# Kernel tuning notes

Measured on AMD Instinct MI355X. Metric: run time of the kernel, lower is better.

## Reference

```python
import jax, jax.numpy as jnp
import numpy as np

V = 500_000
NF = 1_000_000
K_DEG = 7


def _build_mesh_ops(rng):
    faces = rng.integers(0, V, size=(NF, 3), dtype=np.int64)
    f0, f1, f2 = faces[:, 0], faces[:, 1], faces[:, 2]
    rows = np.concatenate([f0, f1, f1, f2, f2, f0])
    cols = np.concatenate([f1, f0, f2, f1, f0, f2])
    keep = rows != cols
    rows, cols = rows[keep], cols[keep]
    code = np.unique(rows * V + cols)  # dedupe symmetric edge list
    rows_u = (code // V).astype(np.int32)
    cols_u = (code % V).astype(np.int32)
    deg = np.bincount(rows_u, minlength=V).astype(np.float32)
    deg = np.maximum(deg, 1.0)
    off_vals = (1.0 / deg[rows_u]).astype(np.float32)
    diag = np.arange(V, dtype=np.int32)
    lap_rows = np.concatenate([rows_u, diag])
    lap_cols = np.concatenate([cols_u, diag])
    lap_vals = np.concatenate([off_vals, -np.ones(V, dtype=np.float32)])
    # sparse hexagon operator K: ~7 nnz per row
    k_rows = np.repeat(np.arange(V, dtype=np.int32), K_DEG)
    k_cols = rng.integers(0, V, size=V * K_DEG).astype(np.int32)
    k_vals = (rng.standard_normal(V * K_DEG) * 0.1).astype(np.float32)
    return faces.astype(np.int32), lap_rows, lap_cols, lap_vals, k_rows, k_cols, k_vals


def setup_inputs() -> dict:
    key = jax.random.key(0)
    rng = np.random.default_rng(0)
    faces, lap_rows, lap_cols, lap_vals, k_rows, k_cols, k_vals = _build_mesh_ops(rng)
    vertices = jax.random.normal(key, (V, 3), dtype=jnp.float32)
    return {
        "vertices": vertices,
        "center": jnp.zeros((1, 3), dtype=jnp.float32),
        "lap_rows": jnp.asarray(lap_rows),
        "lap_cols": jnp.asarray(lap_cols),
        "lap_vals": jnp.asarray(lap_vals),
        "k_rows": jnp.asarray(k_rows),
        "k_cols": jnp.asarray(k_cols),
        "k_vals": jnp.asarray(k_vals),
        "faces": jnp.asarray(faces),
        "total_num": 4,
    }


def _spmv3(rows, cols, vals, verts, n):
    # sparse [n,n] COO matmul with [n,3] verts
    gathered = vals[:, None] * verts[cols]  # [nnz,3]
    return jax.ops.segment_sum(gathered, rows, num_segments=n)


def reference(vertices, center, lap_rows, lap_cols, lap_vals,
              k_rows, k_cols, k_vals, faces, total_num):
    n = vertices.shape[0]
    verts = vertices + center  # [V,3], broadcast of [1,3] center
    # uniform laplacian smoothing loss: mean_i ||(L v)_i||_2
    lap_out = _spmv3(lap_rows, lap_cols, lap_vals, verts, n)
    laplacian_loss = jnp.mean(jnp.linalg.norm(lap_out, axis=1))
    # hexagon regularity loss: mean_i ||(K v)_i||^2
    k_out = _spmv3(k_rows, k_cols, k_vals, verts, n)
    hexagon_loss = jnp.mean(jnp.sum(k_out * k_out, axis=1))
    vertices_rep = jnp.tile(verts[None], (total_num, 1, 1))
    faces_rep = jnp.tile(faces[None], (total_num, 1, 1))
    zero = jnp.zeros((), dtype=verts.dtype)
    return (vertices_rep, faces_rep, laplacian_loss, hexagon_loss, zero, zero)
```

## Files before the change

kernel.cpp:

```cpp
#include <hip/hip_runtime.h>
#include <hip/hip_fp16.h>
#include <math.h>

#define BLK  256
#define KDEG 7
#define CH   8

typedef float fvec4 __attribute__((ext_vector_type(4)));
typedef int   ivec4 __attribute__((ext_vector_type(4)));

__global__ void vrep_kernel(const fvec4* __restrict__ vin,
                            const float* __restrict__ center,
                            fvec4* __restrict__ out,
                            int n4, int T) {
    int i = blockIdx.x * blockDim.x + threadIdx.x;
    if (i >= n4) return;
    float c0 = center[0], c1 = center[1], c2 = center[2];
    fvec4 f = vin[i];
    int m = i % 3;
    float a0 = (m == 0) ? c0 : (m == 1) ? c1 : c2;
    float a1 = (m == 0) ? c1 : (m == 1) ? c2 : c0;
    float a2 = (m == 0) ? c2 : (m == 1) ? c0 : c1;
    f.x += a0; f.y += a1; f.z += a2; f.w += a0;
    for (int t = 0; t < T; ++t)
        __builtin_nontemporal_store(f, &out[(long)t * n4 + i]);
}

__global__ void pack_kernel(const float* __restrict__ vertices,
                            const float* __restrict__ center,
                            ushort4* __restrict__ v16,
                            int* __restrict__ row_start,
                            float* __restrict__ out, long scalar_base, int V) {
    int r = blockIdx.x * blockDim.x + threadIdx.x;
    if (r == 0) {
        out[scalar_base + 0] = 0.f;
        out[scalar_base + 1] = 0.f;
        out[scalar_base + 2] = 0.f;
        out[scalar_base + 3] = 0.f;
    }
    if (r >= V) return;
    long b = (long)r * 3;
    float x = vertices[b]     + center[0];
    float y = vertices[b + 1] + center[1];
    float z = vertices[b + 2] + center[2];
    ushort4 u;
    u.x = __half_as_ushort(__float2half(x));
    u.y = __half_as_ushort(__float2half(y));
    u.z = __half_as_ushort(__float2half(z));
    u.w = 0;
    v16[r] = u;
    row_start[r] = -1;
}

__global__ void frep_kernel(const ivec4* __restrict__ faces,
                            fvec4* __restrict__ out,
                            int n4, int T) {
    int i = blockIdx.x * blockDim.x + threadIdx.x;
    if (i >= n4) return;
    ivec4 f = faces[i];
    fvec4 g;
    g.x = (float)f.x; g.y = (float)f.y; g.z = (float)f.z; g.w = (float)f.w;
    for (int t = 0; t < T; ++t)
        __builtin_nontemporal_store(g, &out[(long)t * n4 + i]);
}

__global__ void row_bounds_kernel(const int* __restrict__ rows,
                                  int* __restrict__ row_start,
                                  int* __restrict__ row_end,
                                  int nnz_off) {
    int j = blockIdx.x * blockDim.x + threadIdx.x;
    if (j >= nnz_off) return;
    int r = rows[j];
    if (j == 0) {
        row_start[r] = 0;
    } else {
        int rp = rows[j - 1];
        if (rp != r) {
            row_start[r] = j;
            row_end[rp] = j;
        }
    }
    if (j == nnz_off - 1) row_end[r] = nnz_off;
}

__device__ __forceinline__ float2 block_reduce_sum2(float2 v) {
    for (int o = 32; o > 0; o >>= 1) {
        v.x += __shfl_down(v.x, o, 64);
        v.y += __shfl_down(v.y, o, 64);
    }
    __shared__ float2 s[BLK / 64];
    int lane = threadIdx.x & 63;
    int wid  = threadIdx.x >> 6;
    if (lane == 0) s[wid] = v;
    __syncthreads();
    if (wid == 0) {
        v = (lane < BLK / 64) ? s[lane] : make_float2(0.f, 0.f);
        for (int o = (BLK / 64) / 2; o > 0; o >>= 1) {
            v.x += __shfl_down(v.x, o, 64);
            v.y += __shfl_down(v.y, o, 64);
        }
    }
    return v;
}

__launch_bounds__(BLK, 6)
__global__ void fused_loss_kernel(const int* __restrict__ row_start,
                                  const int* __restrict__ row_end,
                                  const int* __restrict__ cols,
                                  const int* __restrict__ kcols,
                                  const float* __restrict__ kvals,
                                  const ushort4* __restrict__ v16,
                                  int V, float invV,
                                  float* __restrict__ acc ) {
    const int r   = blockIdx.x * BLK + threadIdx.x;
    const bool act = (r < V);
    const int rr  = act ? r : 0;

    int lo = 0, hi = 0;
    if (act) {
        lo = row_start[r];
        hi = (lo >= 0) ? row_end[r] : 0;
        if (lo < 0) lo = 0;
    }
    const int cnt = hi - lo;

    float qx = 0.f, qy = 0.f, qz = 0.f;
    {
        long kb = (long)rr * KDEG;
        int   kc[KDEG]; float kv[KDEG];
#pragma unroll
        for (int t = 0; t < KDEG; ++t) { kc[t] = kcols[kb + t]; kv[t] = kvals[kb + t]; }
        ushort4 ku[KDEG];
#pragma unroll
        for (int t = 0; t < KDEG; ++t) ku[t] = v16[kc[t]];
#pragma unroll
        for (int t = 0; t < KDEG; ++t) {
            qx += kv[t] * __half2float(__ushort_as_half(ku[t].x));
            qy += kv[t] * __half2float(__ushort_as_half(ku[t].y));
            qz += kv[t] * __half2float(__ushort_as_half(ku[t].z));
        }
    }

    float sx = 0.f, sy = 0.f, sz = 0.f;
    for (int j = lo; j < hi; j += CH) {
        int m = hi - j; if (m > CH) m = CH;
        int cc[CH];
#pragma unroll
        for (int t = 0; t < CH; ++t)
            if (t < m) cc[t] = cols[j + t];
        ushort4 cu[CH];
#pragma unroll
        for (int t = 0; t < CH; ++t)
            if (t < m) cu[t] = v16[cc[t]];
#pragma unroll
        for (int t = 0; t < CH; ++t)
            if (t < m) {
                sx += __half2float(__ushort_as_half(cu[t].x));
                sy += __half2float(__ushort_as_half(cu[t].y));
                sz += __half2float(__ushort_as_half(cu[t].z));
            }
    }

    float2 contrib = make_float2(0.f, 0.f);
    if (act) {
        ushort4 ur = v16[rr];
        float vx = __half2float(__ushort_as_half(ur.x));
        float vy = __half2float(__ushort_as_half(ur.y));
        float vz = __half2float(__ushort_as_half(ur.z));
        float inv = (cnt > 0) ? 1.f / (float)cnt : 0.f;
        float lx = sx * inv - vx;
        float ly = sy * inv - vy;
        float lz = sz * inv - vz;
        contrib.x = sqrtf(lx * lx + ly * ly + lz * lz) * invV;
        contrib.y = (qx * qx + qy * qy + qz * qz) * invV;
    }
    float2 s = block_reduce_sum2(contrib);
    if (threadIdx.x == 0) {
        atomicAdd(&acc[0], s.x);
        atomicAdd(&acc[1], s.y);
    }
}

__global__ void finalize_kernel(float* __restrict__ scal, float invV) {
    scal[0] *= invV;
    scal[1] *= invV;
}

__global__ void vrep_scalar(const float* __restrict__ vertices,
                            const float* __restrict__ center,
                            float* __restrict__ out, int V3, int T) {
    int i = blockIdx.x * blockDim.x + threadIdx.x;
    if (i >= V3) return;
    float v = vertices[i] + center[i % 3];
    for (int t = 0; t < T; ++t) out[(long)t * V3 + i] = v;
}

__global__ void frep_scalar(const int* __restrict__ faces,
                            float* __restrict__ out, int NF3, int T) {
    int i = blockIdx.x * blockDim.x + threadIdx.x;
    if (i >= NF3) return;
    float f = (float)faces[i];
    for (int t = 0; t < T; ++t) out[(long)t * NF3 + i] = f;
}

__global__ void zero_scal_kernel(float* __restrict__ scal) {
    scal[0] = 0.f; scal[1] = 0.f; scal[2] = 0.f; scal[3] = 0.f;
}

__global__ void lap_loss_fb(const int* __restrict__ rows,
                            const int* __restrict__ cols,
                            const float* __restrict__ vals,
                            const float* __restrict__ verts,
                            int nnz_off, int V, float* __restrict__ acc) {
    int r = blockIdx.x * blockDim.x + threadIdx.x;
    float contrib = 0.f;
    if (r < V) {
        int lo = 0, hi = nnz_off;
        while (lo < hi) { int mid = (lo + hi) >> 1; if (rows[mid] < r) lo = mid + 1; else hi = mid; }
        float sx = 0.f, sy = 0.f, sz = 0.f;
        for (int j = lo; j < nnz_off; ++j) {
            if (rows[j] != r) break;
            float v = vals[j]; long c = (long)cols[j] * 3;
            sx += v * verts[c]; sy += v * verts[c + 1]; sz += v * verts[c + 2];
        }
        float dv = vals[nnz_off + r]; long c = (long)r * 3;
        sx += dv * verts[c]; sy += dv * verts[c + 1]; sz += dv * verts[c + 2];
        contrib = sqrtf(sx * sx + sy * sy + sz * sz);
    }
    float2 s = block_reduce_sum2(make_float2(contrib, 0.f));
    if (threadIdx.x == 0) atomicAdd(acc, s.x);
}

__global__ void k_loss_fb(const int* __restrict__ kcols,
                          const float* __restrict__ kvals,
                          const float* __restrict__ verts,
                          int V, int K, float* __restrict__ acc) {
    int r = blockIdx.x * blockDim.x + threadIdx.x;
    float contrib = 0.f;
    if (r < V) {
        long base = (long)r * K;
        float sx = 0.f, sy = 0.f, sz = 0.f;
        for (int j = 0; j < K; ++j) {
            float v = kvals[base + j]; long c = (long)kcols[base + j] * 3;
            sx += v * verts[c]; sy += v * verts[c + 1]; sz += v * verts[c + 2];
        }
        contrib = sx * sx + sy * sy + sz * sz;
    }
    float2 s = block_reduce_sum2(make_float2(contrib, 0.f));
    if (threadIdx.x == 0) atomicAdd(acc, s.x);
}

extern "C" void kernel_launch(void* const* d_in, const int* in_sizes, int n_in,
                              void* d_out, int out_size, void* d_ws, size_t ws_size,
                              hipStream_t stream) {
    const float* vertices = (const float*)d_in[0];
    const float* center   = (const float*)d_in[1];
    const int*   lap_rows = (const int*)d_in[2];
    const int*   lap_cols = (const int*)d_in[3];
    const float* lap_vals = (const float*)d_in[4];
    const int*   k_cols   = (const int*)d_in[6];
    const float* k_vals   = (const float*)d_in[7];
    const int*   faces    = (const int*)d_in[8];

    float* out = (float*)d_out;

    const int V3      = in_sizes[0];
    const int V       = V3 / 3;
    const int nnz     = in_sizes[2];
    const int nnz_off = nnz - V;
    const int K       = in_sizes[7] / V;
    const int NF3     = in_sizes[8];
    const long scalar_base = (long)out_size - 4;
    const int T = (int)(((long)out_size - 4) / ((long)V3 + (long)NF3));

    const size_t need = (size_t)V * (4 + 4 + 8);
    int*     row_start = (int*)d_ws;
    int*     row_end   = row_start + V;
    ushort4* v16       = (ushort4*)(row_end + V);

    const bool fast = (ws_size >= need) && (K == KDEG) &&
                      ((V3 & 3) == 0) && ((NF3 & 3) == 0);

    if (fast) {
        const int n4v = V3 >> 2;
        vrep_kernel<<<(n4v + BLK - 1) / BLK, BLK, 0, stream>>>(
            (const fvec4*)vertices, center, (fvec4*)out, n4v, T);

        pack_kernel<<<(V + BLK - 1) / BLK, BLK, 0, stream>>>(
            vertices, center, v16, row_start, out, scalar_base, V);

        const int n4f = NF3 >> 2;
        frep_kernel<<<(n4f + BLK - 1) / BLK, BLK, 0, stream>>>(
            (const ivec4*)faces, (fvec4*)(out + (long)T * V3), n4f, T);

        row_bounds_kernel<<<(nnz_off + BLK - 1) / BLK, BLK, 0, stream>>>(
            lap_rows, row_start, row_end, nnz_off);

        fused_loss_kernel<<<(V + BLK - 1) / BLK, BLK, 0, stream>>>(
            row_start, row_end, lap_cols, k_cols, k_vals, v16,
            V, 1.0f / (float)V, out + scalar_base);
    } else {
        zero_scal_kernel<<<1, 1, 0, stream>>>(out + scalar_base);
        vrep_scalar<<<(V3 + BLK - 1) / BLK, BLK, 0, stream>>>(
            vertices, center, out, V3, T);
        frep_scalar<<<(NF3 + BLK - 1) / BLK, BLK, 0, stream>>>(
            faces, out + (long)T * V3, NF3, T);
        lap_loss_fb<<<(V + BLK - 1) / BLK, BLK, 0, stream>>>(
            lap_rows, lap_cols, lap_vals, out, nnz_off, V, out + scalar_base);
        k_loss_fb<<<(V + BLK - 1) / BLK, BLK, 0, stream>>>(
            k_cols, k_vals, out, V, K, out + scalar_base + 1);
        finalize_kernel<<<1, 1, 0, stream>>>(out + scalar_base, 1.0f / (float)V);
    }
}
```

Measured before the change: 283.6 us.

## Fuse replication, packing and row-bounds into one grid-stride prep kernel

Merges the vertex replication, fp16 packing, face replication and CSR row-bounds kernels into a single persistent grid-stride kernel with a fixed grid. Row bounds now fill empty rows explicitly, so the -1 initialization and its sentinel check in the loss kernel are dropped. The loss kernel also issues the first chunk of Laplacian column loads together with the K-operator gathers to raise memory-level parallelism. This removes three launches and the inter-kernel serialization, at the cost of a fixed grid size and some serial filling loops for gaps between rows.

```diff
diff --git a/kernel.cpp b/kernel.cpp
--- a/kernel.cpp
+++ b/kernel.cpp
@@ -2,85 +2,84 @@
 #include <hip/hip_fp16.h>
 #include <math.h>
 
-#define BLK  256
-#define KDEG 7
-#define CH   8
+#define BLK   256
+#define KDEG  7
+#define CH    8
+#define PREPB 2048
 
 typedef float fvec4 __attribute__((ext_vector_type(4)));
 typedef int   ivec4 __attribute__((ext_vector_type(4)));
 
-__global__ void vrep_kernel(const fvec4* __restrict__ vin,
+__global__ void prep_kernel(const fvec4* __restrict__ vin4,
+                            const float* __restrict__ vertices,
                             const float* __restrict__ center,
-                            fvec4* __restrict__ out,
-                            int n4, int T) {
-    int i = blockIdx.x * blockDim.x + threadIdx.x;
-    if (i >= n4) return;
-    float c0 = center[0], c1 = center[1], c2 = center[2];
-    fvec4 f = vin[i];
-    int m = i % 3;
-    float a0 = (m == 0) ? c0 : (m == 1) ? c1 : c2;
-    float a1 = (m == 0) ? c1 : (m == 1) ? c2 : c0;
-    float a2 = (m == 0) ? c2 : (m == 1) ? c0 : c1;
-    f.x += a0; f.y += a1; f.z += a2; f.w += a0;
-    for (int t = 0; t < T; ++t)
-        __builtin_nontemporal_store(f, &out[(long)t * n4 + i]);
-}
-
-__global__ void pack_kernel(const float* __restrict__ vertices,
-                            const float* __restrict__ center,
+                            const ivec4* __restrict__ faces4,
+                            const int*  __restrict__ rows,
+                            fvec4* __restrict__ vout4,
+                            fvec4* __restrict__ fout4,
                             ushort4* __restrict__ v16,
                             int* __restrict__ row_start,
-                            float* __restrict__ out, long scalar_base, int V) {
-    int r = blockIdx.x * blockDim.x + threadIdx.x;
-    if (r == 0) {
-        out[scalar_base + 0] = 0.f;
-        out[scalar_base + 1] = 0.f;
-        out[scalar_base + 2] = 0.f;
-        out[scalar_base + 3] = 0.f;
-    }
-    if (r >= V) return;
-    long b = (long)r * 3;
-    float x = vertices[b]     + center[0];
-    float y = vertices[b + 1] + center[1];
-    float z = vertices[b + 2] + center[2];
-    ushort4 u;
-    u.x = __half_as_ushort(__float2half(x));
-    u.y = __half_as_ushort(__float2half(y));
-    u.z = __half_as_ushort(__float2half(z));
-    u.w = 0;
-    v16[r] = u;
-    row_start[r] = -1;
-}
-
-__global__ void frep_kernel(const ivec4* __restrict__ faces,
-                            fvec4* __restrict__ out,
-                            int n4, int T) {
-    int i = blockIdx.x * blockDim.x + threadIdx.x;
-    if (i >= n4) return;
-    ivec4 f = faces[i];
-    fvec4 g;
-    g.x = (float)f.x; g.y = (float)f.y; g.z = (float)f.z; g.w = (float)f.w;
-    for (int t = 0; t < T; ++t)
-        __builtin_nontemporal_store(g, &out[(long)t * n4 + i]);
-}
-
-__global__ void row_bounds_kernel(const int* __restrict__ rows,
-                                  int* __restrict__ row_start,
-                                  int* __restrict__ row_end,
-                                  int nnz_off) {
-    int j = blockIdx.x * blockDim.x + threadIdx.x;
-    if (j >= nnz_off) return;
-    int r = rows[j];
-    if (j == 0) {
-        row_start[r] = 0;
-    } else {
-        int rp = rows[j - 1];
-        if (rp != r) {
-            row_start[r] = j;
-            row_end[rp] = j;
-        }
-    }
-    if (j == nnz_off - 1) row_end[r] = nnz_off;
+                            int* __restrict__ row_end,
+                            float* __restrict__ scal,
+                            int n4v, int n4f, int V, int nnz_off, int T) {
+    const int tid0   = blockIdx.x * BLK + threadIdx.x;
+    const int stride = gridDim.x * BLK;
+    const float c0 = center[0], c1 = center[1], c2 = center[2];
+
+    if (tid0 == 0) {
+        scal[0] = 0.f; scal[1] = 0.f; scal[2] = 0.f; scal[3] = 0.f;
+    }
+
+    for (int i = tid0; i < n4v; i += stride) {
+        fvec4 f = vin4[i];
+        int m = i % 3;
+        float a0 = (m == 0) ? c0 : (m == 1) ? c1 : c2;
+        float a1 = (m == 0) ? c1 : (m == 1) ? c2 : c0;
+        float a2 = (m == 0) ? c2 : (m == 1) ? c0 : c1;
+        f.x += a0; f.y += a1; f.z += a2; f.w += a0;
+        for (int t = 0; t < T; ++t)
+            __builtin_nontemporal_store(f, &vout4[(long)t * n4v + i]);
+    }
+
+    for (int r = tid0; r < V; r += stride) {
+        long b = (long)r * 3;
+        float x = vertices[b]     + c0;
+        float y = vertices[b + 1] + c1;
+        float z = vertices[b + 2] + c2;
+        ushort4 u;
+        u.x = __half_as_ushort(__float2half(x));
+        u.y = __half_as_ushort(__float2half(y));
+        u.z = __half_as_ushort(__float2half(z));
+        u.w = 0;
+        v16[r] = u;
+    }
+
+    for (int i = tid0; i < n4f; i += stride) {
+        ivec4 f = faces4[i];
+        fvec4 g;
+        g.x = (float)f.x; g.y = (float)f.y; g.z = (float)f.z; g.w = (float)f.w;
+        for (int t = 0; t < T; ++t)
+            __builtin_nontemporal_store(g, &fout4[(long)t * n4f + i]);
+    }
+
+    for (int j = tid0; j < nnz_off; j += stride) {
+        int r = rows[j];
+        if (j == 0) {
+            for (int rr = 0; rr < r; ++rr) { row_start[rr] = 0; row_end[rr] = 0; }
+            row_start[r] = 0;
+        } else {
+            int rp = rows[j - 1];
+            if (rp != r) {
+                row_end[rp] = j;
+                for (int rr = rp + 1; rr < r; ++rr) { row_start[rr] = j; row_end[rr] = j; }
+                row_start[r] = j;
+            }
+        }
+        if (j == nnz_off - 1) {
+            row_end[r] = nnz_off;
+            for (int rr = r + 1; rr < V; ++rr) { row_start[rr] = nnz_off; row_end[rr] = nnz_off; }
+        }
+    }
 }
 
 __device__ __forceinline__ float2 block_reduce_sum2(float2 v) {
@@ -112,52 +111,66 @@
                                   const ushort4* __restrict__ v16,
                                   int V, float invV,
                                   float* __restrict__ acc ) {
-    const int r   = blockIdx.x * BLK + threadIdx.x;
+    const int r    = blockIdx.x * BLK + threadIdx.x;
     const bool act = (r < V);
-    const int rr  = act ? r : 0;
-
-    int lo = 0, hi = 0;
-    if (act) {
-        lo = row_start[r];
-        hi = (lo >= 0) ? row_end[r] : 0;
-        if (lo < 0) lo = 0;
-    }
+    const int rr   = act ? r : 0;
+
+    int lo = row_start[rr];
+    int hi = row_end[rr];
+    if (!act) { lo = 0; hi = 0; }
     const int cnt = hi - lo;
 
+    long kb = (long)rr * KDEG;
+    int   kc[KDEG]; float kv[KDEG];
+#pragma unroll
+    for (int t = 0; t < KDEG; ++t) { kc[t] = kcols[kb + t]; kv[t] = kvals[kb + t]; }
+
+    int m0 = cnt < CH ? cnt : CH;
+    int cc[CH];
+#pragma unroll
+    for (int t = 0; t < CH; ++t)
+        if (t < m0) cc[t] = cols[lo + t];
+
+    ushort4 ku[KDEG];
+#pragma unroll
+    for (int t = 0; t < KDEG; ++t) ku[t] = v16[kc[t]];
+    ushort4 cu[CH];
+#pragma unroll
+    for (int t = 0; t < CH; ++t)
+        if (t < m0) cu[t] = v16[cc[t]];
+
     float qx = 0.f, qy = 0.f, qz = 0.f;
-    {
-        long kb = (long)rr * KDEG;
-        int   kc[KDEG]; float kv[KDEG];
-#pragma unroll
-        for (int t = 0; t < KDEG; ++t) { kc[t] = kcols[kb + t]; kv[t] = kvals[kb + t]; }
-        ushort4 ku[KDEG];
-#pragma unroll
-        for (int t = 0; t < KDEG; ++t) ku[t] = v16[kc[t]];
-#pragma unroll
-        for (int t = 0; t < KDEG; ++t) {
-            qx += kv[t] * __half2float(__ushort_as_half(ku[t].x));
-            qy += kv[t] * __half2float(__ushort_as_half(ku[t].y));
-            qz += kv[t] * __half2float(__ushort_as_half(ku[t].z));
-        }
-    }
-
+#pragma unroll
+    for (int t = 0; t < KDEG; ++t) {
+        qx += kv[t] * __half2float(__ushort_as_half(ku[t].x));
+        qy += kv[t] * __half2float(__ushort_as_half(ku[t].y));
+        qz += kv[t] * __half2float(__ushort_as_half(ku[t].z));
+    }
     float sx = 0.f, sy = 0.f, sz = 0.f;
-    for (int j = lo; j < hi; j += CH) {
+#pragma unroll
+    for (int t = 0; t < CH; ++t)
+        if (t < m0) {
+            sx += __half2float(__ushort_as_half(cu[t].x));
+            sy += __half2float(__ushort_as_half(cu[t].y));
+            sz += __half2float(__ushort_as_half(cu[t].z));
+        }
+
+    for (int j = lo + CH; j < hi; j += CH) {
         int m = hi - j; if (m > CH) m = CH;
-        int cc[CH];
+        int c2[CH];
 #pragma unroll
         for (int t = 0; t < CH; ++t)
-            if (t < m) cc[t] = cols[j + t];
-        ushort4 cu[CH];
+            if (t < m) c2[t] = cols[j + t];
+        ushort4 u2[CH];
 #pragma unroll
         for (int t = 0; t < CH; ++t)
-            if (t < m) cu[t] = v16[cc[t]];
+            if (t < m) u2[t] = v16[c2[t]];
 #pragma unroll
         for (int t = 0; t < CH; ++t)
             if (t < m) {
-                sx += __half2float(__ushort_as_half(cu[t].x));
-                sy += __half2float(__ushort_as_half(cu[t].y));
-                sz += __half2float(__ushort_as_half(cu[t].z));
+                sx += __half2float(__ushort_as_half(u2[t].x));
+                sy += __half2float(__ushort_as_half(u2[t].y));
+                sz += __half2float(__ushort_as_half(u2[t].z));
             }
     }
 
@@ -179,11 +192,6 @@
         atomicAdd(&acc[0], s.x);
         atomicAdd(&acc[1], s.y);
     }
-}
-
-__global__ void finalize_kernel(float* __restrict__ scal, float invV) {
-    scal[0] *= invV;
-    scal[1] *= invV;
 }
 
 __global__ void vrep_scalar(const float* __restrict__ vertices,
@@ -250,6 +258,11 @@
     if (threadIdx.x == 0) atomicAdd(acc, s.x);
 }
 
+__global__ void finalize_kernel(float* __restrict__ scal, float invV) {
+    scal[0] *= invV;
+    scal[1] *= invV;
+}
+
 extern "C" void kernel_launch(void* const* d_in, const int* in_sizes, int n_in,
                               void* d_out, int out_size, void* d_ws, size_t ws_size,
                               hipStream_t stream) {
@@ -283,18 +296,13 @@
 
     if (fast) {
         const int n4v = V3 >> 2;
-        vrep_kernel<<<(n4v + BLK - 1) / BLK, BLK, 0, stream>>>(
-            (const fvec4*)vertices, center, (fvec4*)out, n4v, T);
-
-        pack_kernel<<<(V + BLK - 1) / BLK, BLK, 0, stream>>>(
-            vertices, center, v16, row_start, out, scalar_base, V);
-
         const int n4f = NF3 >> 2;
-        frep_kernel<<<(n4f + BLK - 1) / BLK, BLK, 0, stream>>>(
-            (const ivec4*)faces, (fvec4*)(out + (long)T * V3), n4f, T);
-
-        row_bounds_kernel<<<(nnz_off + BLK - 1) / BLK, BLK, 0, stream>>>(
-            lap_rows, row_start, row_end, nnz_off);
+        prep_kernel<<<PREPB, BLK, 0, stream>>>(
+            (const fvec4*)vertices, vertices, center,
+            (const ivec4*)faces, lap_rows,
+            (fvec4*)out, (fvec4*)(out + (long)T * V3),
+            v16, row_start, row_end, out + scalar_base,
+            n4v, n4f, V, nnz_off, T);
 
         fused_loss_kernel<<<(V + BLK - 1) / BLK, BLK, 0, stream>>>(
             row_start, row_end, lap_cols, k_cols, k_vals, v16,
```

Result: no change. 284.9 us (+0.4%).
